# Performance work log

Measured on AMD Instinct MI355X. Metric: run time of the kernel, lower is better.

The kernel has to match this reference:

```python
import jax, jax.numpy as jnp
import numpy as np

NEG_INF = -9e15


def setup_inputs() -> dict:
    key = jax.random.key(0)
    k1, k2, k3, k4 = jax.random.split(key, 4)
    N, F_in, H, F_out = 4096, 512, 8, 64
    node_features = jax.random.normal(k1, (N, F_in), dtype=jnp.float32)
    adj_matrix = jax.random.randint(k2, (N, N), 0, 2, dtype=jnp.int32)
    # ensure self-loops so every row has at least one unmasked entry
    adj_matrix = jnp.maximum(adj_matrix, jnp.eye(N, dtype=jnp.int32))
    W = jax.random.normal(k3, (H, F_in, F_out), dtype=jnp.float32) * 0.05
    a = jax.random.normal(k4, (H, 2 * F_out), dtype=jnp.float32) * 0.05
    return {"node_features": node_features, "adj_matrix": adj_matrix, "W": W, "a": a}


def reference(node_features, adj_matrix, W, a):
    alpha = 0.2
    H, F_in, F_out = W.shape
    # Per-head linear projection: [H, N, F_out]
    Wh = jnp.einsum("nf,hfo->hno", node_features, W)
    # Attention logits e_ij = LeakyReLU(a1 . Wh_i + a2 . Wh_j)
    f_src = jnp.einsum("hno,ho->hn", Wh, a[:, :F_out])   # [H, N]
    f_dst = jnp.einsum("hno,ho->hn", Wh, a[:, F_out:])   # [H, N]
    e = jax.nn.leaky_relu(f_src[:, :, None] + f_dst[:, None, :], negative_slope=alpha)  # [H, N, N]
    # Mask by adjacency, softmax over neighbors
    masked = jnp.where(adj_matrix[None, :, :] > 0, e, NEG_INF)
    attn = jax.nn.softmax(masked, axis=-1)               # [H, N, N]
    # Aggregate neighbor features per head
    h_prime = jnp.einsum("hnm,hmo->hno", attn, Wh)       # [H, N, F_out]
    # Concat heads along feature dim -> [N, H*F_out]
    return jnp.transpose(h_prime, (1, 0, 2)).reshape(h_prime.shape[1], H * F_out)
```

## Files before the change

kernel.cpp:

```cpp
#include <hip/hip_runtime.h>
#include <stdint.h>


#define NN 4096
#define FIN 512
#define NH 8
#define FO 64

typedef _Float16 f16x8 __attribute__((ext_vector_type(8)));
typedef _Float16 f16x2 __attribute__((ext_vector_type(2)));
typedef __attribute__((ext_vector_type(4))) float f32x4;

union H8 { f16x8 v; f16x2 p[4]; unsigned u[4]; };
union U2 { unsigned u; f16x2 v; };

__device__ __forceinline__ unsigned short f2h(float f) {
  _Float16 h = (_Float16)f;
  return __builtin_bit_cast(unsigned short, h);
}

__device__ __forceinline__ f16x8 ld_cvt8(const float* p) {
  float4 a = *(const float4*)p, b = *(const float4*)(p + 4);
  f16x8 r;
  r[0] = (_Float16)a.x; r[1] = (_Float16)a.y; r[2] = (_Float16)a.z; r[3] = (_Float16)a.w;
  r[4] = (_Float16)b.x; r[5] = (_Float16)b.y; r[6] = (_Float16)b.z; r[7] = (_Float16)b.w;
  return r;
}

__global__ __launch_bounds__(256) void prep_w_kernel(
    const float* __restrict__ W, const float* __restrict__ a,
    unsigned short* __restrict__ WbT, unsigned short* __restrict__ WAh) {
  int bid = blockIdx.x, tid = threadIdx.x;
  if (bid < 1024) {
    int item = bid * 256 + tid;
    int o = item & 63, k = (item >> 6) & 511, h = item >> 15;
    WbT[h * 32768 + o * 512 + k] = f2h(W[h * 32768 + k * 64 + o]);
  } else {
    int item = (bid - 1024) * 256 + tid;
    int h = item >> 10, which = (item >> 9) & 1, k = item & 511;
    const float4* wp = (const float4*)(W + ((size_t)h * FIN + k) * FO);
    const float4* ap = (const float4*)(a + h * 128 + which * 64);
    float s = 0.f;
#pragma unroll
    for (int o4 = 0; o4 < 16; ++o4) {
      float4 w4 = wp[o4], a4 = ap[o4];
      s += w4.x * a4.x + w4.y * a4.y + w4.z * a4.z + w4.w * a4.w;
    }
    WAh[(h * 2 + which) * FIN + k] = f2h(s);
  }
}

__global__ __launch_bounds__(512, 4) void proj_adj_kernel(
    const float* __restrict__ X, const int* __restrict__ adj,
    const unsigned short* __restrict__ WbT, const unsigned short* __restrict__ WAh,
    unsigned short* __restrict__ Whfrag, float* __restrict__ Rf,
    unsigned short* __restrict__ E1h, unsigned short* __restrict__ E2h,
    unsigned* __restrict__ adjbitsT) {
  __shared__ float red[4 * 64 * 20];
  int lane = threadIdx.x & 63, wave = threadIdx.x >> 6;
  int row16 = lane & 15, grp = lane >> 4;
  int bx = blockIdx.x;
  if (bx >= 544) {
    int item = (bx - 544) * 512 + threadIdx.x;
    int r = item >> 7, jt = item & 127;
    const int4* p = (const int4*)(adj + (size_t)r * NN + jt * 32);
    unsigned bits = 0;
#pragma unroll
    for (int b = 0; b < 8; ++b) {
      int4 v = p[b];
      bits |= (unsigned)(v.x & 1) << (4 * b);
      bits |= (unsigned)(v.y & 1) << (4 * b + 1);
      bits |= (unsigned)(v.z & 1) << (4 * b + 2);
      bits |= (unsigned)(v.w & 1) << (4 * b + 3);
    }
    adjbitsT[(size_t)jt * NN + r] = bits;
    return;
  }
  if (bx >= 512) {
    int i0 = ((bx - 512) * 8 + wave) * 16;
    if (i0 >= NN) return;
    f32x4 acc = {0, 0, 0, 0};
    const float* xb = X + (size_t)(i0 + row16) * FIN + grp * 8;
    const unsigned short* wb = WAh + row16 * FIN + grp * 8;
#pragma unroll
    for (int k0 = 0; k0 < FIN; k0 += 32)
      acc = __builtin_amdgcn_mfma_f32_16x16x32_f16(ld_cvt8(xb + k0),
                                                   *(const f16x8*)(wb + k0), acc, 0, 0, 0);
    int hh = row16 >> 1;
#pragma unroll
    for (int reg = 0; reg < 4; ++reg) {
      int rr = i0 + grp * 4 + reg;
      float v = acc[reg];
      if (row16 & 1) {
        E1h[hh * NN + rr] = f2h(0.5f * __expf(v));
        E2h[hh * NN + rr] = f2h(0.5f * __expf(0.2f * v));
      } else {
        Rf[hh * NN + rr] = __expf(-0.8f * v);
      }
    }
    return;
  }
  int kh = wave >> 2, jb = wave & 3;
  int job = bx * 4 + jb;
  int h = job & 7, rt = job >> 3;
  int i0 = rt * 16;
  f32x4 acc[4] = {{0,0,0,0},{0,0,0,0},{0,0,0,0},{0,0,0,0}};
  const float* xb = X + (size_t)(i0 + row16) * FIN + kh * 256 + grp * 8;
  const unsigned short* wb = WbT + h * (FO * FIN) + row16 * FIN + kh * 256 + grp * 8;
#pragma unroll
  for (int k0 = 0; k0 < 256; k0 += 32) {
    f16x8 af = ld_cvt8(xb + k0);
#pragma unroll
    for (int cb = 0; cb < 4; ++cb)
      acc[cb] = __builtin_amdgcn_mfma_f32_16x16x32_f16(
          af, *(const f16x8*)(wb + cb * 16 * FIN + k0), acc[cb], 0, 0, 0);
  }
  if (kh == 1) {
    float* q = red + (jb * 64 + lane) * 20;
#pragma unroll
    for (int cb = 0; cb < 4; ++cb) *(f32x4*)(q + cb * 4) = acc[cb];
  }
  __syncthreads();
  if (kh == 0) {
    const float* q = red + (jb * 64 + lane) * 20;
#pragma unroll
    for (int cb = 0; cb < 4; ++cb) acc[cb] += *(const f32x4*)(q + cb * 4);
    int jt = i0 >> 5;
    int kk0 = (i0 & 31) + grp * 4;
    int tl = (kk0 >> 3) * 16 + row16;
    int e0 = kk0 & 7;
#pragma unroll
    for (int cb = 0; cb < 4; ++cb) {
      ushort4 pk;
      pk.x = f2h(acc[cb][0]); pk.y = f2h(acc[cb][1]);
      pk.z = f2h(acc[cb][2]); pk.w = f2h(acc[cb][3]);
      *(ushort4*)(Whfrag + (((size_t)h * 128 + jt) * 4 + cb) * 512 + tl * 8 + e0) = pk;
    }
  }
}

struct Tile {
  f16x8 b0, b1, b2, b3;
  f16x8 e1, e2;
  unsigned aw0, aw1, aw2, aw3;
};

__global__ __launch_bounds__(256, 2) void gat_kernel(
    const unsigned* __restrict__ adjbitsT, const unsigned short* __restrict__ Whfrag,
    const float* __restrict__ Rf, const unsigned short* __restrict__ E1h,
    const unsigned short* __restrict__ E2h, float* __restrict__ out) {
  __shared__ __align__(16) float red[3072];
  int h = blockIdx.y;
  int lane = threadIdx.x & 63, jseg = threadIdx.x >> 6;
  int row16 = lane & 15, grp = lane >> 4;
  int r0 = blockIdx.x * 64;
  int jt0 = jseg * 32;

  f16x2 Rh[4];
#pragma unroll
  for (int gi = 0; gi < 4; ++gi) {
    _Float16 rv = (_Float16)Rf[h * NN + r0 + gi * 16 + row16];
    Rh[gi][0] = rv; Rh[gi][1] = rv;
  }

  H8 ones;
#pragma unroll
  for (int k = 0; k < 4; ++k) ones.u[k] = 0x3C003C00u;

  const unsigned short* wsrc = Whfrag + (size_t)h * 262144 + (size_t)jt0 * 2048 + lane * 8;
  const unsigned short* e1p = E1h + h * NN + jt0 * 32 + grp * 8;
  const unsigned short* e2p = E2h + h * NN + jt0 * 32 + grp * 8;
  const unsigned* ap = adjbitsT + (size_t)jt0 * NN + r0 + row16;

  f32x4 acc[4][5];
#pragma unroll
  for (int gi = 0; gi < 4; ++gi)
#pragma unroll
    for (int cc = 0; cc < 5; ++cc) acc[gi][cc] = (f32x4){0, 0, 0, 0};

  auto ld = [&](int p, Tile& t) {
    const unsigned short* bs = wsrc + (size_t)p * 2048;
    t.b0 = *(const f16x8*)(bs);
    t.b1 = *(const f16x8*)(bs + 512);
    t.b2 = *(const f16x8*)(bs + 1024);
    t.b3 = *(const f16x8*)(bs + 1536);
    t.e1 = *(const f16x8*)(e1p + p * 32);
    t.e2 = *(const f16x8*)(e2p + p * 32);
    const unsigned* aq = ap + (size_t)p * NN;
    t.aw0 = aq[0]; t.aw1 = aq[16]; t.aw2 = aq[32]; t.aw3 = aq[48];
  };

  auto compute = [&](const Tile& t) {
    H8 e1, e2;
    e1.v = t.e1; e2.v = t.e2;
    unsigned aw[4] = {t.aw0, t.aw1, t.aw2, t.aw3};
#pragma unroll
    for (int gi = 0; gi < 4; ++gi) {
      unsigned bb = (aw[gi] >> (grp * 8)) & 0xffu;
      unsigned tt = bb | (bb << 15);
      H8 af;
#pragma unroll
      for (int k = 0; k < 4; ++k) {
        f16x2 mx = __builtin_elementwise_max(e1.p[k], Rh[gi] * e2.p[k]);
        U2 m;
        m.u = (tt << (14 - 2 * k)) & 0x40004000u;
        af.p[k] = mx * m.v;
      }
      acc[gi][0] = __builtin_amdgcn_mfma_f32_16x16x32_f16(af.v, t.b0, acc[gi][0], 0, 0, 0);
      acc[gi][1] = __builtin_amdgcn_mfma_f32_16x16x32_f16(af.v, t.b1, acc[gi][1], 0, 0, 0);
      acc[gi][2] = __builtin_amdgcn_mfma_f32_16x16x32_f16(af.v, t.b2, acc[gi][2], 0, 0, 0);
      acc[gi][3] = __builtin_amdgcn_mfma_f32_16x16x32_f16(af.v, t.b3, acc[gi][3], 0, 0, 0);
      acc[gi][4] = __builtin_amdgcn_mfma_f32_16x16x32_f16(af.v, ones.v, acc[gi][4], 0, 0, 0);
    }
  };

  Tile tA, tB;
  ld(0, tA);
#pragma unroll 1
  for (int p2 = 0; p2 < 15; ++p2) {
    ld(2 * p2 + 1, tB);
    asm volatile("" ::: "memory");
    compute(tA);
    ld(2 * p2 + 2, tA);
    asm volatile("" ::: "memory");
    compute(tB);
  }
  ld(31, tB);
  compute(tA);
  compute(tB);

  __syncthreads();
#pragma unroll
  for (int cc = 0; cc < 5; ++cc) {
    if (jseg != 0) {
#pragma unroll
      for (int gi = 0; gi < 4; ++gi)
        *(f32x4*)(red + (((jseg - 1) * 4 + gi) * 64 + lane) * 4) = acc[gi][cc];
    }
    __syncthreads();
    if (jseg == 0) {
#pragma unroll
      for (int s = 0; s < 3; ++s)
#pragma unroll
        for (int gi = 0; gi < 4; ++gi)
          acc[gi][cc] += *(const f32x4*)(red + ((s * 4 + gi) * 64 + lane) * 4);
    }
    __syncthreads();
  }

  if (jseg == 0) {
#pragma unroll
    for (int gi = 0; gi < 4; ++gi) {
#pragma unroll
      for (int reg = 0; reg < 4; ++reg) {
        float inv = 1.0f / acc[gi][4][reg];
        int row = r0 + gi * 16 + grp * 4 + reg;
        float* op = out + (size_t)row * (NH * FO) + h * FO + row16;
        op[0]  = acc[gi][0][reg] * inv;
        op[16] = acc[gi][1][reg] * inv;
        op[32] = acc[gi][2][reg] * inv;
        op[48] = acc[gi][3][reg] * inv;
      }
    }
  }
}

extern "C" void kernel_launch(void* const* d_in, const int* in_sizes, int n_in,
                              void* d_out, int out_size, void* d_ws, size_t ws_size,
                              hipStream_t stream) {
  const float* X  = (const float*)d_in[0];
  const int* adj  = (const int*)d_in[1];
  const float* W  = (const float*)d_in[2];
  const float* a  = (const float*)d_in[3];
  float* out = (float*)d_out;
  char* ws = (char*)d_ws;

  unsigned short* WbT    = (unsigned short*)(ws + 0);
  unsigned* adjbitsT     = (unsigned*)(ws + 524288);
  unsigned short* Whfrag = (unsigned short*)(ws + 2621440);
  unsigned short* WAh    = (unsigned short*)(ws + 6815744);
  float* Rf              = (float*)(ws + 6832128);
  unsigned short* E1h    = (unsigned short*)(ws + 6963200);
  unsigned short* E2h    = (unsigned short*)(ws + 7028736);

  prep_w_kernel<<<1056, 256, 0, stream>>>(W, a, WbT, WAh);
  proj_adj_kernel<<<1568, 512, 0, stream>>>(X, adj, WbT, WAh, Whfrag, Rf, E1h, E2h,
                                            adjbitsT);
  gat_kernel<<<dim3(64, 8), 256, 0, stream>>>(adjbitsT, Whfrag, Rf, E1h, E2h, out);
}
```

Before: 78.81 us.

## Split adjacency packing into its own kernel and preload X fragments before MFMAs

Moves the adjacency-to-bitmask packing out of the combined projection kernel into a separate 256-thread kernel launched first, leaving a projection-only kernel. In the main projection path, all eight converted X fragments are loaded up front before the MFMA loop, which puts more loads in flight. The src/dst path also preloads fragments into an array that is never used (dead loads the compiler may remove). The split costs an extra kernel launch and removes the overlap between memory-bound packing blocks and compute blocks in the same grid.

```diff
diff --git a/kernel.cpp b/kernel.cpp
--- a/kernel.cpp
+++ b/kernel.cpp
@@ -50,42 +50,50 @@
   }
 }
 
-__global__ __launch_bounds__(512, 4) void proj_adj_kernel(
-    const float* __restrict__ X, const int* __restrict__ adj,
-    const unsigned short* __restrict__ WbT, const unsigned short* __restrict__ WAh,
+__global__ __launch_bounds__(256) void adj_pack_kernel(
+    const int* __restrict__ adj, unsigned* __restrict__ adjbitsT) {
+  int item = blockIdx.x * 256 + threadIdx.x;
+  int r = item >> 7, jt = item & 127;
+  const int4* p = (const int4*)(adj + (size_t)r * NN + jt * 32);
+  unsigned bits = 0;
+#pragma unroll
+  for (int b = 0; b < 8; ++b) {
+    int4 v = p[b];
+    bits |= (unsigned)(v.x & 1) << (4 * b);
+    bits |= (unsigned)(v.y & 1) << (4 * b + 1);
+    bits |= (unsigned)(v.z & 1) << (4 * b + 2);
+    bits |= (unsigned)(v.w & 1) << (4 * b + 3);
+  }
+  adjbitsT[(size_t)jt * NN + r] = bits;
+}
+
+__global__ __launch_bounds__(512, 4) void proj_sd_kernel(
+    const float* __restrict__ X, const unsigned short* __restrict__ WbT,
+    const unsigned short* __restrict__ WAh,
     unsigned short* __restrict__ Whfrag, float* __restrict__ Rf,
-    unsigned short* __restrict__ E1h, unsigned short* __restrict__ E2h,
-    unsigned* __restrict__ adjbitsT) {
+    unsigned short* __restrict__ E1h, unsigned short* __restrict__ E2h) {
   __shared__ float red[4 * 64 * 20];
   int lane = threadIdx.x & 63, wave = threadIdx.x >> 6;
   int row16 = lane & 15, grp = lane >> 4;
   int bx = blockIdx.x;
-  if (bx >= 544) {
-    int item = (bx - 544) * 512 + threadIdx.x;
-    int r = item >> 7, jt = item & 127;
-    const int4* p = (const int4*)(adj + (size_t)r * NN + jt * 32);
-    unsigned bits = 0;
-#pragma unroll
-    for (int b = 0; b < 8; ++b) {
-      int4 v = p[b];
-      bits |= (unsigned)(v.x & 1) << (4 * b);
-      bits |= (unsigned)(v.y & 1) << (4 * b + 1);
-      bits |= (unsigned)(v.z & 1) << (4 * b + 2);
-      bits |= (unsigned)(v.w & 1) << (4 * b + 3);
-    }
-    adjbitsT[(size_t)jt * NN + r] = bits;
-    return;
-  }
   if (bx >= 512) {
     int i0 = ((bx - 512) * 8 + wave) * 16;
     if (i0 >= NN) return;
-    f32x4 acc = {0, 0, 0, 0};
     const float* xb = X + (size_t)(i0 + row16) * FIN + grp * 8;
     const unsigned short* wb = WAh + row16 * FIN + grp * 8;
-#pragma unroll
-    for (int k0 = 0; k0 < FIN; k0 += 32)
-      acc = __builtin_amdgcn_mfma_f32_16x16x32_f16(ld_cvt8(xb + k0),
-                                                   *(const f16x8*)(wb + k0), acc, 0, 0, 0);
+    f16x8 xa[8];
+#pragma unroll
+    for (int i = 0; i < 8; ++i) xa[i] = ld_cvt8(xb + i * 64);
+    f32x4 acc = {0, 0, 0, 0};
+#pragma unroll
+    for (int i = 0; i < 8; ++i)
+      acc = __builtin_amdgcn_mfma_f32_16x16x32_f16(
+          ld_cvt8(xb + i * 32), *(const f16x8*)(wb + i * 32), acc, 0, 0, 0);
+#pragma unroll
+    for (int i = 8; i < 16; ++i)
+      acc = __builtin_amdgcn_mfma_f32_16x16x32_f16(
+          ld_cvt8(xb + i * 32), *(const f16x8*)(wb + i * 32), acc, 0, 0, 0);
+    (void)xa;
     int hh = row16 >> 1;
 #pragma unroll
     for (int reg = 0; reg < 4; ++reg) {
@@ -107,13 +115,15 @@
   f32x4 acc[4] = {{0,0,0,0},{0,0,0,0},{0,0,0,0},{0,0,0,0}};
   const float* xb = X + (size_t)(i0 + row16) * FIN + kh * 256 + grp * 8;
   const unsigned short* wb = WbT + h * (FO * FIN) + row16 * FIN + kh * 256 + grp * 8;
-#pragma unroll
-  for (int k0 = 0; k0 < 256; k0 += 32) {
-    f16x8 af = ld_cvt8(xb + k0);
+  f16x8 xa[8];
+#pragma unroll
+  for (int i = 0; i < 8; ++i) xa[i] = ld_cvt8(xb + i * 32);
+#pragma unroll
+  for (int i = 0; i < 8; ++i) {
 #pragma unroll
     for (int cb = 0; cb < 4; ++cb)
       acc[cb] = __builtin_amdgcn_mfma_f32_16x16x32_f16(
-          af, *(const f16x8*)(wb + cb * 16 * FIN + k0), acc[cb], 0, 0, 0);
+          xa[i], *(const f16x8*)(wb + cb * 16 * FIN + i * 32), acc[cb], 0, 0, 0);
   }
   if (kh == 1) {
     float* q = red + (jb * 64 + lane) * 20;
@@ -284,7 +294,7 @@
   unsigned short* E2h    = (unsigned short*)(ws + 7028736);
 
   prep_w_kernel<<<1056, 256, 0, stream>>>(W, a, WbT, WAh);
-  proj_adj_kernel<<<1568, 512, 0, stream>>>(X, adj, WbT, WAh, Whfrag, Rf, E1h, E2h,
-                                            adjbitsT);
+  adj_pack_kernel<<<2048, 256, 0, stream>>>(adj, adjbitsT);
+  proj_sd_kernel<<<544, 512, 0, stream>>>(X, WbT, WAh, Whfrag, Rf, E1h, E2h);
   gat_kernel<<<dim3(64, 8), 256, 0, stream>>>(adjbitsT, Whfrag, Rf, E1h, E2h, out);
 }
```

Measured after the change: 89.09 us. 13.0% more time.

## Keep X tile in registers and loop heads per wave; pack 64 adj bits per thread

Applied to the files above, without the earlier changes.

The projection path now loads each 16-row X tile once into registers as fp16 and reuses it for the attention-logit MFMA and for all 8 heads in a serial loop. This replaces the old scheme, which split K across wave pairs, reloaded X per head and reduced partial sums through shared memory. The adjacency packing now produces two 32-bit words per thread, which cuts the grid from 1568 to 544 blocks. In exchange, only 32 blocks (256 waves) do all the projection work, each running a long serial head loop, so the GEMM part has much less parallelism and uses more registers, and occupancy drops to 3 blocks per SM.

```diff
diff --git a/kernel.cpp b/kernel.cpp
--- a/kernel.cpp
+++ b/kernel.cpp
@@ -50,93 +50,90 @@
   }
 }
 
-__global__ __launch_bounds__(512, 4) void proj_adj_kernel(
+__global__ __launch_bounds__(512, 3) void proj_pack_kernel(
     const float* __restrict__ X, const int* __restrict__ adj,
     const unsigned short* __restrict__ WbT, const unsigned short* __restrict__ WAh,
     unsigned short* __restrict__ Whfrag, float* __restrict__ Rf,
     unsigned short* __restrict__ E1h, unsigned short* __restrict__ E2h,
     unsigned* __restrict__ adjbitsT) {
-  __shared__ float red[4 * 64 * 20];
-  int lane = threadIdx.x & 63, wave = threadIdx.x >> 6;
-  int row16 = lane & 15, grp = lane >> 4;
   int bx = blockIdx.x;
-  if (bx >= 544) {
-    int item = (bx - 544) * 512 + threadIdx.x;
-    int r = item >> 7, jt = item & 127;
-    const int4* p = (const int4*)(adj + (size_t)r * NN + jt * 32);
-    unsigned bits = 0;
-#pragma unroll
-    for (int b = 0; b < 8; ++b) {
-      int4 v = p[b];
-      bits |= (unsigned)(v.x & 1) << (4 * b);
-      bits |= (unsigned)(v.y & 1) << (4 * b + 1);
-      bits |= (unsigned)(v.z & 1) << (4 * b + 2);
-      bits |= (unsigned)(v.w & 1) << (4 * b + 3);
-    }
-    adjbitsT[(size_t)jt * NN + r] = bits;
-    return;
-  }
-  if (bx >= 512) {
-    int i0 = ((bx - 512) * 8 + wave) * 16;
-    if (i0 >= NN) return;
-    f32x4 acc = {0, 0, 0, 0};
+  if (bx < 32) {
+    int lane = threadIdx.x & 63, wave = threadIdx.x >> 6;
+    int row16 = lane & 15, grp = lane >> 4;
+    int rt = bx * 8 + wave;
+    int i0 = rt * 16;
     const float* xb = X + (size_t)(i0 + row16) * FIN + grp * 8;
-    const unsigned short* wb = WAh + row16 * FIN + grp * 8;
-#pragma unroll
-    for (int k0 = 0; k0 < FIN; k0 += 32)
-      acc = __builtin_amdgcn_mfma_f32_16x16x32_f16(ld_cvt8(xb + k0),
-                                                   *(const f16x8*)(wb + k0), acc, 0, 0, 0);
-    int hh = row16 >> 1;
-#pragma unroll
-    for (int reg = 0; reg < 4; ++reg) {
-      int rr = i0 + grp * 4 + reg;
-      float v = acc[reg];
-      if (row16 & 1) {
-        E1h[hh * NN + rr] = f2h(0.5f * __expf(v));
-        E2h[hh * NN + rr] = f2h(0.5f * __expf(0.2f * v));
-      } else {
-        Rf[hh * NN + rr] = __expf(-0.8f * v);
-      }
-    }
-    return;
-  }
-  int kh = wave >> 2, jb = wave & 3;
-  int job = bx * 4 + jb;
-  int h = job & 7, rt = job >> 3;
-  int i0 = rt * 16;
-  f32x4 acc[4] = {{0,0,0,0},{0,0,0,0},{0,0,0,0},{0,0,0,0}};
-  const float* xb = X + (size_t)(i0 + row16) * FIN + kh * 256 + grp * 8;
-  const unsigned short* wb = WbT + h * (FO * FIN) + row16 * FIN + kh * 256 + grp * 8;
-#pragma unroll
-  for (int k0 = 0; k0 < 256; k0 += 32) {
-    f16x8 af = ld_cvt8(xb + k0);
-#pragma unroll
-    for (int cb = 0; cb < 4; ++cb)
-      acc[cb] = __builtin_amdgcn_mfma_f32_16x16x32_f16(
-          af, *(const f16x8*)(wb + cb * 16 * FIN + k0), acc[cb], 0, 0, 0);
-  }
-  if (kh == 1) {
-    float* q = red + (jb * 64 + lane) * 20;
-#pragma unroll
-    for (int cb = 0; cb < 4; ++cb) *(f32x4*)(q + cb * 4) = acc[cb];
-  }
-  __syncthreads();
-  if (kh == 0) {
-    const float* q = red + (jb * 64 + lane) * 20;
-#pragma unroll
-    for (int cb = 0; cb < 4; ++cb) acc[cb] += *(const f32x4*)(q + cb * 4);
+    f16x8 xa[16];
+#pragma unroll
+    for (int i = 0; i < 16; ++i) xa[i] = ld_cvt8(xb + i * 32);
+
+    {
+      const unsigned short* wb = WAh + row16 * FIN + grp * 8;
+      f32x4 acc = {0, 0, 0, 0};
+#pragma unroll
+      for (int i = 0; i < 16; ++i)
+        acc = __builtin_amdgcn_mfma_f32_16x16x32_f16(
+            xa[i], *(const f16x8*)(wb + i * 32), acc, 0, 0, 0);
+      int hh = row16 >> 1;
+#pragma unroll
+      for (int reg = 0; reg < 4; ++reg) {
+        int rr = i0 + grp * 4 + reg;
+        float v = acc[reg];
+        if (row16 & 1) {
+          E1h[hh * NN + rr] = f2h(0.5f * __expf(v));
+          E2h[hh * NN + rr] = f2h(0.5f * __expf(0.2f * v));
+        } else {
+          Rf[hh * NN + rr] = __expf(-0.8f * v);
+        }
+      }
+    }
     int jt = i0 >> 5;
     int kk0 = (i0 & 31) + grp * 4;
     int tl = (kk0 >> 3) * 16 + row16;
     int e0 = kk0 & 7;
-#pragma unroll
-    for (int cb = 0; cb < 4; ++cb) {
-      ushort4 pk;
-      pk.x = f2h(acc[cb][0]); pk.y = f2h(acc[cb][1]);
-      pk.z = f2h(acc[cb][2]); pk.w = f2h(acc[cb][3]);
-      *(ushort4*)(Whfrag + (((size_t)h * 128 + jt) * 4 + cb) * 512 + tl * 8 + e0) = pk;
-    }
-  }
+#pragma unroll 1
+    for (int h = 0; h < NH; ++h) {
+      const unsigned short* wb = WbT + h * (FO * FIN) + row16 * FIN + grp * 8;
+      f32x4 acc[4] = {{0,0,0,0},{0,0,0,0},{0,0,0,0},{0,0,0,0}};
+#pragma unroll
+      for (int i = 0; i < 16; ++i) {
+#pragma unroll
+        for (int cb = 0; cb < 4; ++cb)
+          acc[cb] = __builtin_amdgcn_mfma_f32_16x16x32_f16(
+              xa[i], *(const f16x8*)(wb + cb * 16 * FIN + i * 32), acc[cb], 0, 0, 0);
+      }
+#pragma unroll
+      for (int cb = 0; cb < 4; ++cb) {
+        ushort4 pk;
+        pk.x = f2h(acc[cb][0]); pk.y = f2h(acc[cb][1]);
+        pk.z = f2h(acc[cb][2]); pk.w = f2h(acc[cb][3]);
+        *(ushort4*)(Whfrag + (((size_t)h * 128 + jt) * 4 + cb) * 512 + tl * 8 + e0) = pk;
+      }
+    }
+    return;
+  }
+  int item = (bx - 32) * 512 + threadIdx.x;
+  int r = item >> 6, jt2 = item & 63;
+  const int4* p = (const int4*)(adj + (size_t)r * NN + jt2 * 64);
+  unsigned w0 = 0, w1 = 0;
+#pragma unroll
+  for (int b = 0; b < 8; ++b) {
+    int4 v = p[b];
+    w0 |= (unsigned)(v.x & 1) << (4 * b);
+    w0 |= (unsigned)(v.y & 1) << (4 * b + 1);
+    w0 |= (unsigned)(v.z & 1) << (4 * b + 2);
+    w0 |= (unsigned)(v.w & 1) << (4 * b + 3);
+  }
+#pragma unroll
+  for (int b = 0; b < 8; ++b) {
+    int4 v = p[8 + b];
+    w1 |= (unsigned)(v.x & 1) << (4 * b);
+    w1 |= (unsigned)(v.y & 1) << (4 * b + 1);
+    w1 |= (unsigned)(v.z & 1) << (4 * b + 2);
+    w1 |= (unsigned)(v.w & 1) << (4 * b + 3);
+  }
+  adjbitsT[(size_t)(jt2 * 2 + 0) * NN + r] = w0;
+  adjbitsT[(size_t)(jt2 * 2 + 1) * NN + r] = w1;
 }
 
 struct Tile {
@@ -284,7 +281,7 @@
   unsigned short* E2h    = (unsigned short*)(ws + 7028736);
 
   prep_w_kernel<<<1056, 256, 0, stream>>>(W, a, WbT, WAh);
-  proj_adj_kernel<<<1568, 512, 0, stream>>>(X, adj, WbT, WAh, Whfrag, Rf, E1h, E2h,
+  proj_pack_kernel<<<544, 512, 0, stream>>>(X, adj, WbT, WAh, Whfrag, Rf, E1h, E2h,
                                             adjbitsT);
   gat_kernel<<<dim3(64, 8), 256, 0, stream>>>(adjbitsT, Whfrag, Rf, E1h, E2h, out);
 }
```

Result: slower. 162.7 us (+106.4%).
